# Kernel optimization log

Hardware: AMD Instinct MI355X
Metric: run time of the kernel (lower is better)

## Reference

```python
import jax, jax.numpy as jnp
import numpy as np

N = 8192
F_IN = 256
F_OUT = 256
S = 128          # state_dim
D_INNER = 512    # int(2.0 * out_features)


def _ln(x, g, b, eps=1e-5):
    m = x.mean(-1, keepdims=True)
    v = ((x - m) ** 2).mean(-1, keepdims=True)
    return (x - m) / jnp.sqrt(v + eps) * g + b


def setup_inputs() -> dict:
    key = jax.random.key(0)
    ks = jax.random.split(key, 20)
    s = 0.05
    d = {}
    d['h'] = jax.random.normal(ks[0], (N, F_IN), dtype=jnp.float32)
    d['adj'] = jax.random.randint(ks[1], (N, N), 0, 2, dtype=jnp.int32)
    d['W'] = jax.random.normal(ks[2], (F_IN, F_OUT), dtype=jnp.float32) * s
    d['a_src'] = jax.random.normal(ks[3], (F_OUT, 1), dtype=jnp.float32) * s
    d['a_dst'] = jax.random.normal(ks[4], (F_OUT, 1), dtype=jnp.float32) * s
    d['W_bcdt'] = jax.random.normal(ks[5], (F_OUT, 3 * S), dtype=jnp.float32) * s
    d['b_bcdt'] = jnp.zeros((3 * S,), jnp.float32)
    d['abp_w'] = jax.random.normal(ks[6], (S, F_OUT), dtype=jnp.float32) * s
    d['abp_b'] = jnp.zeros((F_OUT,), jnp.float32)
    d['cp_w'] = jax.random.normal(ks[7], (S, 1), dtype=jnp.float32) * s
    d['cp_b'] = jnp.zeros((1,), jnp.float32)
    d['W_hz'] = jax.random.normal(ks[8], (F_OUT, 2 * D_INNER), dtype=jnp.float32) * s
    d['b_hz'] = jnp.zeros((2 * D_INNER,), jnp.float32)
    d['out_w'] = jax.random.normal(ks[9], (D_INNER, F_OUT), dtype=jnp.float32) * s
    d['out_b'] = jnp.zeros((F_OUT,), jnp.float32)
    d['fe1_w'] = jax.random.normal(ks[10], (F_OUT, D_INNER), dtype=jnp.float32) * s
    d['fe1_b'] = jnp.zeros((D_INNER,), jnp.float32)
    d['fe_ln_g'] = jnp.ones((D_INNER,), jnp.float32)
    d['fe_ln_b'] = jnp.zeros((D_INNER,), jnp.float32)
    d['fe2_w'] = jax.random.normal(ks[11], (D_INNER, F_OUT), dtype=jnp.float32) * s
    d['fe2_b'] = jnp.zeros((F_OUT,), jnp.float32)
    d['A'] = jax.random.uniform(ks[12], (S,), minval=1.0, maxval=64.0, dtype=jnp.float32)
    d['D'] = jnp.ones((1,), jnp.float32)
    d['g1_w'] = jax.random.normal(ks[13], (2 * F_OUT, 2 * F_OUT), dtype=jnp.float32) * s
    d['g1_b'] = jnp.zeros((2 * F_OUT,), jnp.float32)
    d['g_ln_g'] = jnp.ones((2 * F_OUT,), jnp.float32)
    d['g_ln_b'] = jnp.zeros((2 * F_OUT,), jnp.float32)
    d['g2_w'] = jax.random.normal(ks[14], (2 * F_OUT, F_OUT), dtype=jnp.float32) * s
    d['g2_b'] = jnp.zeros((F_OUT,), jnp.float32)
    d['ln_g'] = jnp.ones((F_OUT,), jnp.float32)
    d['ln_b'] = jnp.zeros((F_OUT,), jnp.float32)
    return d


def reference(h, adj, W, a_src, a_dst, W_bcdt, b_bcdt, abp_w, abp_b, cp_w, cp_b,
              W_hz, b_hz, out_w, out_b, fe1_w, fe1_b, fe_ln_g, fe_ln_b, fe2_w,
              fe2_b, A, D, g1_w, g1_b, g_ln_g, g_ln_b, g2_w, g2_b, ln_g, ln_b):
    Wh = h @ W                                   # [N, F_OUT]
    # GAT-style masked attention
    e = Wh @ a_src + (Wh @ a_dst).T              # [N, N]
    e = jnp.where(e > 0, e, 0.2 * e)             # leaky_relu(0.2)
    e = jnp.where(adj > 0, e, jnp.float32(-9e15))
    attn = jax.nn.softmax(e, axis=1)
    h_attn = attn @ Wh                           # [N, F_OUT]
    # feature enhancer
    h_enh = jax.nn.silu(_ln(Wh @ fe1_w + fe1_b, fe_ln_g, fe_ln_b)) @ fe2_w + fe2_b
    # SSM-like branch
    BCdt = Wh @ W_bcdt + b_bcdt                  # [N, 3S]
    B, C, dt = jnp.split(BCdt, 3, axis=1)
    Asm = jax.nn.softmax(dt + A[None, :], axis=1)
    ab = (Asm * B) @ abp_w + abp_b               # [N, F_OUT]
    hs = Wh * ab
    hz = hs @ W_hz + b_hz                        # [N, 2*D_INNER]
    h_part, z = jnp.split(hz, 2, axis=1)
    hs = (h_part * jax.nn.silu(z) + h_part * D) @ out_w + out_b
    c_proj = C @ cp_w + cp_b                     # [N, 1]
    hs = hs * (1.0 + c_proj)
    # gated fusion
    comb = jnp.concatenate([h_attn, hs], axis=1)  # [N, 2*F_OUT]
    g = jax.nn.sigmoid(jax.nn.silu(_ln(comb @ g1_w + g1_b, g_ln_g, g_ln_b)) @ g2_w + g2_b)
    fused = g * h_attn + (1.0 - g) * hs + h_enh
    return _ln(fused, ln_g, ln_b)
```

## Files before the change

kernel.cpp:

```cpp
#include <hip/hip_runtime.h>
#include <cstdint>

typedef __attribute__((ext_vector_type(8))) short short8;
typedef __attribute__((ext_vector_type(4))) float f32x4;

#define DEVINL static __device__ __forceinline__

DEVINL ushort f2b(float f) {
    uint32_t u = __builtin_bit_cast(uint32_t, f);
    u += 0x7FFFu + ((u >> 16) & 1u);
    return (ushort)(u >> 16);
}

typedef __attribute__((address_space(3))) uint32_t lds_u32;
typedef const __attribute__((address_space(1))) uint32_t glb_u32;

DEVINL void load_lds_16(const ushort* g, ushort* l) {
    __builtin_amdgcn_global_load_lds((glb_u32*)g, (lds_u32*)l, 16, 0, 0);
}

constexpr int EPI_F32      = 0;
constexpr int EPI_MUL_BF16 = 2;
constexpr int EPI_SCALE_FB = 3;

template<int K, int EPI>
DEVINL void gemm_k_dev(
    const ushort* __restrict__ A, const ushort* __restrict__ BT,
    const float* __restrict__ bias, int N,
    float* __restrict__ outf, ushort* __restrict__ outb, int obld, int oboff,
    const float* __restrict__ extra, int bx, int by,
    ushort* Asm, ushort* Bsm)
{
    const int wave = threadIdx.x >> 6;
    const int lane = threadIdx.x & 63;
    const int quad = lane >> 4, l16 = lane & 15;
    const int lr = lane >> 3, ls = lane & 7;
    const int m0 = bx * 64, n0 = by * 64;

    f32x4 zero = {0.f, 0.f, 0.f, 0.f};
    f32x4 acc[4] = {zero, zero, zero, zero};

    for (int k0 = 0; k0 < K; k0 += 64) {
        #pragma unroll
        for (int p = 0; p < 2; ++p) {
            const int r = wave * 16 + p * 8 + lr;
            load_lds_16(A + (size_t)(m0 + r) * K + k0 + ((ls ^ (r & 7)) * 8),
                        Asm + (size_t)(wave * 16 + p * 8) * 64);
            load_lds_16(BT + (size_t)(n0 + r) * K + k0 + ((ls ^ (r & 7)) * 8),
                        Bsm + (size_t)(wave * 16 + p * 8) * 64);
        }
        __syncthreads();
        #pragma unroll
        for (int ks = 0; ks < 2; ++ks) {
            const int sl = ((ks * 4 + quad) ^ (l16 & 7)) * 8;
            short8 af = *(const short8*)(Asm + (wave * 16 + l16) * 64 + sl);
            #pragma unroll
            for (int c = 0; c < 4; ++c) {
                short8 bf = *(const short8*)(Bsm + (c * 16 + l16) * 64 + sl);
                acc[c] = __builtin_amdgcn_mfma_f32_16x16x32_bf16(af, bf, acc[c], 0, 0, 0);
            }
        }
        __syncthreads();
    }

    #pragma unroll
    for (int r = 0; r < 4; ++r) {
        const int row = m0 + wave * 16 + quad * 4 + r;
        #pragma unroll
        for (int c = 0; c < 4; ++c) {
            const int col = n0 + c * 16 + l16;
            float v = acc[c][r] + (bias ? bias[col] : 0.f);
            if (EPI == EPI_MUL_BF16) v *= extra[(size_t)row * N + col];
            if (EPI == EPI_SCALE_FB) v *= extra[row];
            if (EPI == EPI_F32 || EPI == EPI_SCALE_FB)
                outf[(size_t)row * N + col] = v;
            if (EPI == EPI_MUL_BF16 || EPI == EPI_SCALE_FB)
                outb[(size_t)row * obld + oboff + col] = f2b(v);
        }
    }
}

__global__ __launch_bounds__(256) void gemm_wh_kernel(
    const ushort* __restrict__ A, const ushort* __restrict__ BT,
    const float* __restrict__ asrc, const float* __restrict__ adst,
    float* __restrict__ Wh, ushort* __restrict__ Whbf, ushort* __restrict__ WhF,
    float* __restrict__ sOut, float* __restrict__ dOut)
{
    __shared__ ushort smem[2 * 64 * 64];
    ushort* Asm = smem;
    ushort* Bsm = smem + 4096;
    constexpr int K = 256;

    const int tid = threadIdx.x;
    const int wave = tid >> 6, lane = tid & 63;
    const int quad = lane >> 4, l16 = lane & 15;
    const int lr = lane >> 3, ls = lane & 7;
    const int m0 = blockIdx.x * 64, n0 = blockIdx.y * 64;

    f32x4 zero = {0.f, 0.f, 0.f, 0.f};
    f32x4 acc[4] = {zero, zero, zero, zero};

    for (int k0 = 0; k0 < K; k0 += 64) {
        #pragma unroll
        for (int p = 0; p < 2; ++p) {
            const int r = wave * 16 + p * 8 + lr;
            load_lds_16(A + (size_t)(m0 + r) * K + k0 + ((ls ^ (r & 7)) * 8),
                        Asm + (size_t)(wave * 16 + p * 8) * 64);
            load_lds_16(BT + (size_t)(n0 + r) * K + k0 + ((ls ^ (r & 7)) * 8),
                        Bsm + (size_t)(wave * 16 + p * 8) * 64);
        }
        __syncthreads();
        #pragma unroll
        for (int ks = 0; ks < 2; ++ks) {
            const int sl = ((ks * 4 + quad) ^ (l16 & 7)) * 8;
            short8 af = *(const short8*)(Asm + (wave * 16 + l16) * 64 + sl);
            #pragma unroll
            for (int c = 0; c < 4; ++c) {
                short8 bf = *(const short8*)(Bsm + (c * 16 + l16) * 64 + sl);
                acc[c] = __builtin_amdgcn_mfma_f32_16x16x32_bf16(af, bf, acc[c], 0, 0, 0);
            }
        }
        __syncthreads();
    }

    ushort* Tsm = smem;
    #pragma unroll
    for (int r = 0; r < 4; ++r) {
        const int rl = wave * 16 + quad * 4 + r;
        const int row = m0 + rl;
        float sp = 0.f, dp = 0.f;
        #pragma unroll
        for (int c = 0; c < 4; ++c) {
            const int cl = c * 16 + l16;
            const int col = n0 + cl;
            const float v = acc[c][r];
            Wh[(size_t)row * 256 + col] = v;
            const ushort b = f2b(v);
            Whbf[(size_t)row * 256 + col] = b;
            Tsm[cl * 72 + rl] = b;
            sp += v * asrc[col]; dp += v * adst[col];
        }
        #pragma unroll
        for (int o = 1; o < 16; o <<= 1) {
            sp += __shfl_xor(sp, o);
            dp += __shfl_xor(dp, o);
        }
        if (l16 == 0) {
            atomicAdd(&sOut[row], sp);
            atomicAdd(&dOut[row], dp);
        }
    }
    __syncthreads();
    const int jb0 = m0 >> 5, fb0 = n0 >> 4;
    #pragma unroll
    for (int jbl = 0; jbl < 2; ++jbl) {
        uint4 v = *(const uint4*)(Tsm + (wave * 16 + l16) * 72 + jbl * 32 + quad * 8);
        *(uint4*)(WhF + ((size_t)((jb0 + jbl) * 16 + fb0 + wave) * 64 + lane) * 8) = v;
    }
}

constexpr int EPR_LNSILU = 0;
constexpr int EPR_BCDT   = 1;
constexpr int EPR_HZ     = 2;
constexpr int EPR_FINAL  = 3;

template<int K, int N, int EPI>
DEVINL void gemm_row_dev(
    const ushort* __restrict__ A, const ushort* __restrict__ BT,
    const float* __restrict__ bias,
    float* __restrict__ outf, ushort* __restrict__ outb,
    const float* __restrict__ q0, const float* __restrict__ q1,
    const float* __restrict__ q2, const float* __restrict__ q3,
    const float* __restrict__ q4,
    int bx, int by, ushort* Asm, ushort* Bsm, float* red)
{
    constexpr int NW = N / 4;
    constexpr int NF = NW / 16;

    const int wave = threadIdx.x >> 6;
    const int lane = threadIdx.x & 63;
    const int quad = lane >> 4, l16 = lane & 15;
    const int lr = lane >> 3, ls = lane & 7;
    const int m0 = bx * 16;
    const ushort* Bb = BT + (EPI == EPR_HZ ? (size_t)by * 512 * K : 0);

    f32x4 zero = {0.f, 0.f, 0.f, 0.f};
    f32x4 acc[NF];
    #pragma unroll
    for (int c = 0; c < NF; ++c) acc[c] = zero;

    for (int k0 = 0; k0 < K; k0 += 64) {
        if (wave < 2) {
            const int r = wave * 8 + lr;
            load_lds_16(A + (size_t)(m0 + r) * K + k0 + ((ls ^ (r & 7)) * 8),
                        Asm + (size_t)(wave * 8) * 64);
        }
        #pragma unroll
        for (int p = 0; p < NW / 8; ++p) {
            const int n = wave * NW + p * 8 + lr;
            load_lds_16(Bb + (size_t)n * K + k0 + ((ls ^ (n & 7)) * 8),
                        Bsm + (size_t)(wave * NW + p * 8) * 64);
        }
        __syncthreads();
        #pragma unroll
        for (int ks = 0; ks < 2; ++ks) {
            const int sl = ((ks * 4 + quad) ^ (l16 & 7)) * 8;
            short8 af = *(const short8*)(Asm + l16 * 64 + sl);
            #pragma unroll
            for (int c = 0; c < NF; ++c) {
                const int gf = (EPI == EPR_BCDT) ? (wave + 4 * c) : (wave * NF + c);
                short8 bf = *(const short8*)(Bsm + (gf * 16 + l16) * 64 + sl);
                acc[c] = __builtin_amdgcn_mfma_f32_16x16x32_bf16(af, bf, acc[c], 0, 0, 0);
            }
        }
        __syncthreads();
    }

    if constexpr (EPI != EPR_HZ) {
        #pragma unroll
        for (int c = 0; c < NF; ++c) {
            const int gf = (EPI == EPR_BCDT) ? (wave + 4 * c) : (wave * NF + c);
            const float bs = bias[gf * 16 + l16];
            #pragma unroll
            for (int r = 0; r < 4; ++r) acc[c][r] += bs;
        }
    }

    if constexpr (EPI == EPR_LNSILU) {
        float s[4], q[4];
        #pragma unroll
        for (int r = 0; r < 4; ++r) {
            s[r] = 0.f; q[r] = 0.f;
            #pragma unroll
            for (int c = 0; c < NF; ++c) { const float v = acc[c][r]; s[r] += v; q[r] += v * v; }
            #pragma unroll
            for (int o = 1; o < 16; o <<= 1) { s[r] += __shfl_xor(s[r], o); q[r] += __shfl_xor(q[r], o); }
        }
        if (l16 == 0) {
            #pragma unroll
            for (int r = 0; r < 4; ++r) {
                red[(quad * 4 + r) * 8 + wave * 2]     = s[r];
                red[(quad * 4 + r) * 8 + wave * 2 + 1] = q[r];
            }
        }
        __syncthreads();
        #pragma unroll
        for (int r = 0; r < 4; ++r) {
            const int row16 = quad * 4 + r;
            float S = 0.f, Q = 0.f;
            #pragma unroll
            for (int w = 0; w < 4; ++w) { S += red[row16 * 8 + w * 2]; Q += red[row16 * 8 + w * 2 + 1]; }
            const float mean = S * (1.f / N);
            const float rstd = rsqrtf(Q * (1.f / N) - mean * mean + 1e-5f);
            #pragma unroll
            for (int c = 0; c < NF; ++c) {
                const int col = (wave * NF + c) * 16 + l16;
                const float y = (acc[c][r] - mean) * rstd * q0[col] + q1[col];
                outb[(size_t)(m0 + row16) * N + col] = f2b(y / (1.f + __expf(-y)));
            }
        }
    } else if constexpr (EPI == EPR_BCDT) {
        float t[2][4], e[2][4];
        #pragma unroll
        for (int ci = 0; ci < 2; ++ci) {
            const int dcol = (wave + 4 * (ci + 4)) * 16 - 256 + l16;
            const float av = q0[dcol];
            #pragma unroll
            for (int r = 0; r < 4; ++r) t[ci][r] = acc[ci + 4][r] + av;
        }
        float pm[4];
        #pragma unroll
        for (int r = 0; r < 4; ++r) {
            pm[r] = fmaxf(t[0][r], t[1][r]);
            #pragma unroll
            for (int o = 1; o < 16; o <<= 1) pm[r] = fmaxf(pm[r], __shfl_xor(pm[r], o));
        }
        if (l16 == 0) {
            #pragma unroll
            for (int r = 0; r < 4; ++r) red[(quad * 4 + r) * 4 + wave] = pm[r];
        }
        __syncthreads();
        float mx[4];
        #pragma unroll
        for (int r = 0; r < 4; ++r) {
            const int row16 = quad * 4 + r;
            mx[r] = fmaxf(fmaxf(red[row16 * 4], red[row16 * 4 + 1]),
                          fmaxf(red[row16 * 4 + 2], red[row16 * 4 + 3]));
        }
        float pe[4], pc2[4];
        #pragma unroll
        for (int r = 0; r < 4; ++r) {
            e[0][r] = __expf(t[0][r] - mx[r]);
            e[1][r] = __expf(t[1][r] - mx[r]);
            pe[r] = e[0][r] + e[1][r];
            pc2[r] = 0.f;
            #pragma unroll
            for (int ci = 0; ci < 2; ++ci) {
                const int ccol = (wave + 4 * (ci + 2)) * 16 - 128 + l16;
                pc2[r] += acc[ci + 2][r] * q1[ccol];
            }
            #pragma unroll
            for (int o = 1; o < 16; o <<= 1) { pe[r] += __shfl_xor(pe[r], o); pc2[r] += __shfl_xor(pc2[r], o); }
        }
        if (l16 == 0) {
            #pragma unroll
            for (int r = 0; r < 4; ++r) {
                red[64  + (quad * 4 + r) * 4 + wave] = pe[r];
                red[128 + (quad * 4 + r) * 4 + wave] = pc2[r];
            }
        }
        __syncthreads();
        #pragma unroll
        for (int r = 0; r < 4; ++r) {
            const int row16 = quad * 4 + r;
            const float inv = 1.f / (red[64 + row16 * 4] + red[64 + row16 * 4 + 1] +
                                     red[64 + row16 * 4 + 2] + red[64 + row16 * 4 + 3]);
            #pragma unroll
            for (int ci = 0; ci < 2; ++ci) {
                const int bcol = (wave + 4 * ci) * 16 + l16;
                outb[(size_t)(m0 + row16) * 128 + bcol] = f2b(acc[ci][r] * e[ci][r] * inv);
            }
        }
        if (wave == 0 && l16 == 0) {
            #pragma unroll
            for (int r = 0; r < 4; ++r) {
                const int row16 = quad * 4 + r;
                outf[m0 + row16] = 1.f + red[128 + row16 * 4] + red[128 + row16 * 4 + 1] +
                                   red[128 + row16 * 4 + 2] + red[128 + row16 * 4 + 3] + q2[0];
            }
        }
    } else if constexpr (EPI == EPR_HZ) {
        float* ep = (float*)Bsm;
        const float D0 = q0[0];
        if (wave >= 2) {
            #pragma unroll
            for (int c = 0; c < NF; ++c) {
                const int lc = (wave * NF + c) * 16 + l16;
                const float bz = bias[512 + by * 256 + lc - 256];
                #pragma unroll
                for (int r = 0; r < 4; ++r) {
                    const float z = acc[c][r] + bz;
                    ep[(quad * 4 + r) * 256 + lc - 256] = z / (1.f + __expf(-z)) + D0;
                }
            }
        }
        __syncthreads();
        if (wave < 2) {
            #pragma unroll
            for (int c = 0; c < NF; ++c) {
                const int lc = (wave * NF + c) * 16 + l16;
                const float bh = bias[by * 256 + lc];
                #pragma unroll
                for (int r = 0; r < 4; ++r) {
                    const float v = (acc[c][r] + bh) * ep[(quad * 4 + r) * 256 + lc];
                    outb[(size_t)(m0 + quad * 4 + r) * 512 + by * 256 + lc] = f2b(v);
                }
            }
        }
    } else {
        float fv[NF][4], s[4], q[4];
        #pragma unroll
        for (int r = 0; r < 4; ++r) { s[r] = 0.f; q[r] = 0.f; }
        #pragma unroll
        for (int c = 0; c < NF; ++c) {
            const int col = (wave * NF + c) * 16 + l16;
            #pragma unroll
            for (int r = 0; r < 4; ++r) {
                const size_t idx = (size_t)(m0 + quad * 4 + r) * 256 + col;
                const float g = 1.f / (1.f + __expf(-acc[c][r]));
                const float f = g * q0[idx] + (1.f - g) * q1[idx] + q2[idx];
                fv[c][r] = f; s[r] += f; q[r] += f * f;
            }
        }
        #pragma unroll
        for (int r = 0; r < 4; ++r) {
            #pragma unroll
            for (int o = 1; o < 16; o <<= 1) { s[r] += __shfl_xor(s[r], o); q[r] += __shfl_xor(q[r], o); }
        }
        if (l16 == 0) {
            #pragma unroll
            for (int r = 0; r < 4; ++r) {
                red[(quad * 4 + r) * 8 + wave * 2]     = s[r];
                red[(quad * 4 + r) * 8 + wave * 2 + 1] = q[r];
            }
        }
        __syncthreads();
        #pragma unroll
        for (int r = 0; r < 4; ++r) {
            const int row16 = quad * 4 + r;
            float S = 0.f, Q = 0.f;
            #pragma unroll
            for (int w = 0; w < 4; ++w) { S += red[row16 * 8 + w * 2]; Q += red[row16 * 8 + w * 2 + 1]; }
            const float mean = S * (1.f / 256.f);
            const float rstd = rsqrtf(Q * (1.f / 256.f) - mean * mean + 1e-5f);
            #pragma unroll
            for (int c = 0; c < NF; ++c) {
                const int col = (wave * NF + c) * 16 + l16;
                outf[(size_t)(m0 + row16) * 256 + col] = (fv[c][r] - mean) * rstd * q3[col] + q4[col];
            }
        }
    }
}

__global__ __launch_bounds__(256) void attn_kernel(
    const int* __restrict__ adj, const float* __restrict__ sA,
    const float* __restrict__ dA, const ushort* __restrict__ WhF,
    float* __restrict__ Upart, float* __restrict__ lpart)
{
    const int tid  = threadIdx.x;
    const int wave = tid >> 6, lane = tid & 63, quad = lane >> 4, l16 = lane & 15;
    const int i0 = blockIdx.x * 64;
    const int js = blockIdx.y;
    const int jbase = js * 2048;
    const int jb0 = jbase >> 5;
    const int rt = wave & 1, ch = wave >> 1;
    const int rr = lane >> 2, jg = lane & 3;
    const int row0 = i0 + rt * 32 + rr;
    const int row1 = row0 + 16;
    const float s0 = sA[row0], s1 = sA[row1];
    const int* adj0 = adj + (size_t)row0 * 8192 + jbase + jg * 8;
    const int* adj1 = adj + (size_t)row1 * 8192 + jbase + jg * 8;
    const float* dAp = dA + jbase + jg * 8;
    const int perm = ((l16 << 2) | quad) << 2;

    f32x4 zero = {0.f, 0.f, 0.f, 0.f};
    f32x4 acc[2][8] = {{zero, zero, zero, zero, zero, zero, zero, zero},
                       {zero, zero, zero, zero, zero, zero, zero, zero}};
    float ls0 = 0.f, ls1 = 0.f;

    #pragma unroll 2
    for (int cb = 0; cb < 64; ++cb) {
        const int off = cb * 32;
        const float4 d0 = *(const float4*)(dAp + off);
        const float4 d1 = *(const float4*)(dAp + off + 4);
        const int4 a00 = *(const int4*)(adj0 + off);
        const int4 a01 = *(const int4*)(adj0 + off + 4);
        const int4 a10 = *(const int4*)(adj1 + off);
        const int4 a11 = *(const int4*)(adj1 + off + 4);
        const float dd[8] = {d0.x, d0.y, d0.z, d0.w, d1.x, d1.y, d1.z, d1.w};
        const int aa0[8] = {a00.x, a00.y, a00.z, a00.w, a01.x, a01.y, a01.z, a01.w};
        const int aa1[8] = {a10.x, a10.y, a10.z, a10.w, a11.x, a11.y, a11.z, a11.w};
        ushort us0[8], us1[8];
        #pragma unroll
        for (int q = 0; q < 8; ++q) {
            float e0 = s0 + dd[q];
            e0 = fmaxf(e0, 0.2f * e0);
            const float w0 = aa0[q] ? __expf(e0) : 0.f;
            ls0 += w0; us0[q] = f2b(w0);
            float e1 = s1 + dd[q];
            e1 = fmaxf(e1, 0.2f * e1);
            const float w1 = aa1[q] ? __expf(e1) : 0.f;
            ls1 += w1; us1[q] = f2b(w1);
        }
        union FR { int d[4]; short8 v; } f0, f1;
        #pragma unroll
        for (int d = 0; d < 4; ++d) {
            const int p0 = (int)((uint)us0[2 * d] | ((uint)us0[2 * d + 1] << 16));
            const int p1 = (int)((uint)us1[2 * d] | ((uint)us1[2 * d + 1] << 16));
            f0.d[d] = __builtin_amdgcn_ds_bpermute(perm, p0);
            f1.d[d] = __builtin_amdgcn_ds_bpermute(perm, p1);
        }
        const ushort* Bp = WhF + ((size_t)((jb0 + cb) * 16 + ch * 8) * 64 + lane) * 8;
        #pragma unroll
        for (int c = 0; c < 8; ++c) {
            short8 bf = *(const short8*)(Bp + (size_t)c * 64 * 8);
            acc[0][c] = __builtin_amdgcn_mfma_f32_16x16x32_bf16(f0.v, bf, acc[0][c], 0, 0, 0);
            acc[1][c] = __builtin_amdgcn_mfma_f32_16x16x32_bf16(f1.v, bf, acc[1][c], 0, 0, 0);
        }
    }

    ls0 += __shfl_down(ls0, 1); ls0 += __shfl_down(ls0, 2);
    ls1 += __shfl_down(ls1, 1); ls1 += __shfl_down(ls1, 2);
    if (ch == 0 && jg == 0) {
        lpart[(size_t)js * 8192 + row0] = ls0;
        lpart[(size_t)js * 8192 + row1] = ls1;
    }

    #pragma unroll
    for (int it = 0; it < 2; ++it) {
        #pragma unroll
        for (int c = 0; c < 8; ++c) {
            const int col = ch * 128 + c * 16 + l16;
            #pragma unroll
            for (int r = 0; r < 4; ++r) {
                const int row = i0 + rt * 32 + it * 16 + quad * 4 + r;
                Upart[((size_t)js * 8192 + row) * 256 + col] = acc[it][c][r];
            }
        }
    }
}

__global__ __launch_bounds__(256) void post_attn_kernel(
    const float* __restrict__ Upart, const float* __restrict__ lpart,
    float* __restrict__ hattn, ushort* __restrict__ comb,
    const ushort* __restrict__ Whbf,
    const ushort* __restrict__ fe1T, const float* __restrict__ fe1_b,
    const float* __restrict__ fe_ln_g, const float* __restrict__ fe_ln_b,
    ushort* __restrict__ tact,
    const ushort* __restrict__ bcdtT, const float* __restrict__ b_bcdt,
    const float* __restrict__ Avec, const float* __restrict__ cpw,
    const float* __restrict__ cpb,
    ushort* __restrict__ SB, float* __restrict__ cscl)
{
    __shared__ ushort Asm[16 * 64];
    __shared__ ushort Bsm[512 * 64];
    __shared__ float red[192];
    const int b = blockIdx.x;

    if (b < 2048) {
        const int row = b * 4 + (threadIdx.x >> 6);
        const int lane = threadIdx.x & 63;
        float l = 0.f;
        #pragma unroll
        for (int js = 0; js < 4; ++js) l += lpart[(size_t)js * 8192 + row];
        const float inv = 1.f / l;
        float4 u = {0.f, 0.f, 0.f, 0.f};
        #pragma unroll
        for (int js = 0; js < 4; ++js) {
            const float4 t = *(const float4*)&Upart[((size_t)js * 8192 + row) * 256 + lane * 4];
            u.x += t.x; u.y += t.y; u.z += t.z; u.w += t.w;
        }
        u.x *= inv; u.y *= inv; u.z *= inv; u.w *= inv;
        *(float4*)&hattn[(size_t)row * 256 + lane * 4] = u;
        union { ushort us[4]; uint2 v; } pk;
        pk.us[0] = f2b(u.x); pk.us[1] = f2b(u.y); pk.us[2] = f2b(u.z); pk.us[3] = f2b(u.w);
        *(uint2*)&comb[(size_t)row * 512 + lane * 4] = pk.v;
    } else if (b < 2560) {
        gemm_row_dev<256, 512, EPR_LNSILU>(Whbf, fe1T, fe1_b, nullptr, tact,
            fe_ln_g, fe_ln_b, nullptr, nullptr, nullptr, b - 2048, 0, Asm, Bsm, red);
    } else {
        gemm_row_dev<256, 384, EPR_BCDT>(Whbf, bcdtT, b_bcdt, cscl, SB,
            Avec, cpw, cpb, nullptr, nullptr, b - 2560, 0, Asm, Bsm, red);
    }
}

__global__ __launch_bounds__(256) void gemm_fe2_sb_kernel(
    const ushort* __restrict__ tact, const ushort* __restrict__ fe2T,
    const float* __restrict__ fe2_b, float* __restrict__ henh,
    const ushort* __restrict__ SB, const ushort* __restrict__ abpT,
    const float* __restrict__ abp_b, ushort* __restrict__ hsbf,
    const float* __restrict__ Wh)
{
    __shared__ ushort Asm[64 * 64];
    __shared__ ushort Bsm[64 * 64];
    const int b = blockIdx.x;
    if (b < 512)
        gemm_k_dev<512, EPI_F32>(tact, fe2T, fe2_b, 256, henh, nullptr, 0, 0,
                                 nullptr, b & 127, b >> 7, Asm, Bsm);
    else
        gemm_k_dev<128, EPI_MUL_BF16>(SB, abpT, abp_b, 256, nullptr, hsbf, 256, 0,
                                      Wh, (b - 512) & 127, (b - 512) >> 7, Asm, Bsm);
}

__global__ __launch_bounds__(256) void gemm_hz_kernel(
    const ushort* __restrict__ hsbf, const ushort* __restrict__ hzT,
    const float* __restrict__ b_hz, ushort* __restrict__ vbf,
    const float* __restrict__ Dvec)
{
    __shared__ ushort Asm[16 * 64];
    __shared__ ushort Bsm[512 * 64];
    __shared__ float red[192];
    gemm_row_dev<256, 512, EPR_HZ>(hsbf, hzT, b_hz, nullptr, vbf, Dvec,
        nullptr, nullptr, nullptr, nullptr, blockIdx.x, blockIdx.y, Asm, Bsm, red);
}

__global__ __launch_bounds__(256) void gemm_out_kernel(
    const ushort* __restrict__ vbf, const ushort* __restrict__ outT,
    const float* __restrict__ out_b, float* __restrict__ hs2,
    ushort* __restrict__ comb, const float* __restrict__ cscl)
{
    __shared__ ushort Asm[64 * 64];
    __shared__ ushort Bsm[64 * 64];
    gemm_k_dev<512, EPI_SCALE_FB>(vbf, outT, out_b, 256, hs2, comb, 512, 256,
                                  cscl, blockIdx.x, blockIdx.y, Asm, Bsm);
}

__global__ __launch_bounds__(256) void gemm_g1_kernel(
    const ushort* __restrict__ comb, const ushort* __restrict__ g1T,
    const float* __restrict__ g1_b, ushort* __restrict__ tact,
    const float* __restrict__ g_ln_g, const float* __restrict__ g_ln_b)
{
    __shared__ ushort Asm[16 * 64];
    __shared__ ushort Bsm[512 * 64];
    __shared__ float red[192];
    gemm_row_dev<512, 512, EPR_LNSILU>(comb, g1T, g1_b, nullptr, tact,
        g_ln_g, g_ln_b, nullptr, nullptr, nullptr, blockIdx.x, 0, Asm, Bsm, red);
}

__global__ __launch_bounds__(256) void gemm_final_kernel(
    const ushort* __restrict__ tact, const ushort* __restrict__ g2T,
    const float* __restrict__ g2_b, float* __restrict__ outp,
    const float* __restrict__ hattn, const float* __restrict__ hs2,
    const float* __restrict__ henh, const float* __restrict__ ln_g,
    const float* __restrict__ ln_b)
{
    __shared__ ushort Asm[16 * 64];
    __shared__ ushort Bsm[256 * 64];
    __shared__ float red[192];
    gemm_row_dev<512, 256, EPR_FINAL>(tact, g2T, g2_b, outp, nullptr,
        hattn, hs2, henh, ln_g, ln_b, blockIdx.x, 0, Asm, Bsm, red);
}

struct TJob { const float* in; ushort* out; int R, C, off, perm; };
struct TArgs { TJob j[10]; };

DEVINL int hzperm(int j) {
    return (j < 512) ? ((j >> 8) << 9) + (j & 255)
                     : (((j - 512) >> 8) << 9) + 256 + ((j - 512) & 255);
}

__global__ __launch_bounds__(256) void multi_transpose_kernel(TArgs a)
{
    __shared__ float tile[32][33];
    const int b = blockIdx.x;
    int ji = 0;
    #pragma unroll
    for (int k = 1; k < 10; ++k) if (b >= a.j[k].off) ji = k;
    const TJob J = a.j[ji];
    const int t = b - J.off;

    if (J.R == 0) {
        const int base = t * 1024 + threadIdx.x;
        #pragma unroll
        for (int k = 0; k < 4; ++k)
            J.out[base + k * 256] = f2b(J.in[base + k * 256]);
        return;
    }
    const int CB = J.C >> 5;
    const int bx = t % CB, by = t / CB;
    const int tx = threadIdx.x & 31, ty = threadIdx.x >> 5;
    const int c0 = bx * 32, r0 = by * 32;
    #pragma unroll
    for (int i = ty; i < 32; i += 8)
        tile[i][tx] = J.in[(size_t)(r0 + i) * J.C + (c0 + tx)];
    __syncthreads();
    #pragma unroll
    for (int i = ty; i < 32; i += 8) {
        int orow = c0 + i;
        if (J.perm) orow = hzperm(orow);
        J.out[(size_t)orow * J.R + (r0 + tx)] = f2b(tile[tx][i]);
    }
}

extern "C" void kernel_launch(void* const* d_in, const int* in_sizes, int n_in,
                              void* d_out, int out_size, void* d_ws, size_t ws_size,
                              hipStream_t stream)
{
    const float* h      = (const float*)d_in[0];
    const int*   adj    = (const int*)  d_in[1];
    const float* W      = (const float*)d_in[2];
    const float* a_src  = (const float*)d_in[3];
    const float* a_dst  = (const float*)d_in[4];
    const float* W_bcdt = (const float*)d_in[5];
    const float* b_bcdt = (const float*)d_in[6];
    const float* abp_w  = (const float*)d_in[7];
    const float* abp_b  = (const float*)d_in[8];
    const float* cp_w   = (const float*)d_in[9];
    const float* cp_b   = (const float*)d_in[10];
    const float* W_hz   = (const float*)d_in[11];
    const float* b_hz   = (const float*)d_in[12];
    const float* out_w  = (const float*)d_in[13];
    const float* out_b  = (const float*)d_in[14];
    const float* fe1_w  = (const float*)d_in[15];
    const float* fe1_b  = (const float*)d_in[16];
    const float* fe_ln_g= (const float*)d_in[17];
    const float* fe_ln_b= (const float*)d_in[18];
    const float* fe2_w  = (const float*)d_in[19];
    const float* fe2_b  = (const float*)d_in[20];
    const float* Avec   = (const float*)d_in[21];
    const float* Dvec   = (const float*)d_in[22];
    const float* g1_w   = (const float*)d_in[23];
    const float* g1_b   = (const float*)d_in[24];
    const float* g_ln_g = (const float*)d_in[25];
    const float* g_ln_b = (const float*)d_in[26];
    const float* g2_w   = (const float*)d_in[27];
    const float* g2_b   = (const float*)d_in[28];
    const float* ln_g   = (const float*)d_in[29];
    const float* ln_b   = (const float*)d_in[30];
    float* outp = (float*)d_out;

    char* p = (char*)d_ws;
    size_t off = 0;
    auto take = [&](size_t nbytes) -> void* {
        void* r = p + off;
        off += (nbytes + 255) & ~(size_t)255;
        return r;
    };
    ushort* wT    = (ushort*)take(256 * 256 * 2);
    ushort* fe1T  = (ushort*)take(512 * 256 * 2);
    ushort* fe2T  = (ushort*)take(256 * 512 * 2);
    ushort* bcdtT = (ushort*)take(384 * 256 * 2);
    ushort* hzT   = (ushort*)take(1024 * 256 * 2);
    ushort* outT  = (ushort*)take(256 * 512 * 2);
    ushort* g1T   = (ushort*)take(512 * 512 * 2);
    ushort* g2T   = (ushort*)take(256 * 512 * 2);
    ushort* abpT  = (ushort*)take(256 * 128 * 2);
    ushort* hbf   = (ushort*)take((size_t)8192 * 256 * 2);
    float*  Wh    = (float*) take((size_t)8192 * 256 * 4);
    ushort* Whbf  = (ushort*)take((size_t)8192 * 256 * 2);
    ushort* WhF   = (ushort*)take((size_t)8192 * 256 * 2);
    float*  sbuf  = (float*) take(8192 * 4);
    float*  dbuf  = (float*) take(8192 * 4);
    float*  cscl  = (float*) take(8192 * 4);
    float*  hattn = (float*) take((size_t)8192 * 256 * 4);
    float*  henh  = (float*) take((size_t)8192 * 256 * 4);
    float*  lpart = (float*) take(4 * 8192 * 4);
    ushort* SB    = (ushort*)take((size_t)8192 * 128 * 2);
    ushort* hsbf  = (ushort*)take((size_t)8192 * 256 * 2);
    ushort* vbf   = (ushort*)take((size_t)8192 * 512 * 2);
    float*  hs2   = (float*) take((size_t)8192 * 256 * 4);
    ushort* comb  = (ushort*)take((size_t)8192 * 512 * 2);
    ushort* tact  = (ushort*)take((size_t)8192 * 512 * 2);
    float*  Upart = (float*) take((size_t)4 * 8192 * 256 * 4);

    (void)in_sizes; (void)n_in; (void)out_size; (void)ws_size;

    hipMemsetAsync(sbuf, 0, 2 * 8192 * sizeof(float), stream);

    {
        TArgs ta; int boff = 0;
        auto addT = [&](int i, const float* in, ushort* out, int R, int C, int perm) {
            ta.j[i] = TJob{in, out, R, C, boff, perm};
            boff += (R / 32) * (C / 32);
        };
        addT(0, W,      wT,    256, 256,  0);
        addT(1, fe1_w,  fe1T,  256, 512,  0);
        addT(2, fe2_w,  fe2T,  512, 256,  0);
        addT(3, W_bcdt, bcdtT, 256, 384,  0);
        addT(4, abp_w,  abpT,  128, 256,  0);
        addT(5, W_hz,   hzT,   256, 1024, 1);
        addT(6, out_w,  outT,  512, 256,  0);
        addT(7, g1_w,   g1T,   512, 512,  0);
        addT(8, g2_w,   g2T,   512, 256,  0);
        ta.j[9] = TJob{h, hbf, 0, 8192 * 256, boff, 0};
        boff += (8192 * 256) / 1024;
        multi_transpose_kernel<<<boff, 256, 0, stream>>>(ta);
    }

    gemm_wh_kernel<<<dim3(128, 4), 256, 0, stream>>>(
        hbf, wT, a_src, a_dst, Wh, Whbf, WhF, sbuf, dbuf);

    attn_kernel<<<dim3(128, 4), 256, 0, stream>>>(adj, sbuf, dbuf, WhF, Upart, lpart);

    post_attn_kernel<<<3072, 256, 0, stream>>>(
        Upart, lpart, hattn, comb, Whbf,
        fe1T, fe1_b, fe_ln_g, fe_ln_b, tact,
        bcdtT, b_bcdt, Avec, cp_w, cp_b, SB, cscl);

    gemm_fe2_sb_kernel<<<1024, 256, 0, stream>>>(
        tact, fe2T, fe2_b, henh, SB, abpT, abp_b, hsbf, Wh);

    gemm_hz_kernel<<<dim3(512, 2), 256, 0, stream>>>(hsbf, hzT, b_hz, vbf, Dvec);

    gemm_out_kernel<<<dim3(128, 4), 256, 0, stream>>>(vbf, outT, out_b, hs2, comb, cscl);

    gemm_g1_kernel<<<512, 256, 0, stream>>>(comb, g1T, g1_b, tact, g_ln_g, g_ln_b);

    gemm_final_kernel<<<512, 256, 0, stream>>>(
        tact, g2T, g2_b, outp, hattn, hs2, henh, ln_g, ln_b);
}
```

Measured before the change: 614.5 us.

## Co-schedule attention with fe1/BCdt GEMMs and store attention partials in bf16

Attention blocks now run in the same launch as the independent fe1 and BCdt row GEMMs, interleaved by block index, so the adjacency-bound attention work can overlap with compute-bound GEMM work. The partial-sum reduction moves into the following fe2/SB kernel. Per-split attention partial accumulators are written as bf16 instead of fp32, halving that intermediate traffic. The cost is reduced precision in the partial sums and a larger static LDS footprint for the attention blocks, which may lower occupancy.

Measured after the change: 676.7 us. 1.1x slower.

```diff
diff --git a/kernel.cpp b/kernel.cpp
--- a/kernel.cpp
+++ b/kernel.cpp
@@ -10,6 +10,10 @@
     uint32_t u = __builtin_bit_cast(uint32_t, f);
     u += 0x7FFFu + ((u >> 16) & 1u);
     return (ushort)(u >> 16);
+}
+DEVINL float b2f(ushort u) {
+    uint32_t x = (uint32_t)u << 16;
+    return __builtin_bit_cast(float, x);
 }
 
 typedef __attribute__((address_space(3))) uint32_t lds_u32;
@@ -402,15 +406,15 @@
     }
 }
 
-__global__ __launch_bounds__(256) void attn_kernel(
+DEVINL void attn_dev(
     const int* __restrict__ adj, const float* __restrict__ sA,
     const float* __restrict__ dA, const ushort* __restrict__ WhF,
-    float* __restrict__ Upart, float* __restrict__ lpart)
+    ushort* __restrict__ Upart, float* __restrict__ lpart,
+    int bx, int js)
 {
     const int tid  = threadIdx.x;
     const int wave = tid >> 6, lane = tid & 63, quad = lane >> 4, l16 = lane & 15;
-    const int i0 = blockIdx.x * 64;
-    const int js = blockIdx.y;
+    const int i0 = bx * 64;
     const int jbase = js * 2048;
     const int jb0 = jbase >> 5;
     const int rt = wave & 1, ch = wave >> 1;
@@ -484,15 +488,16 @@
             #pragma unroll
             for (int r = 0; r < 4; ++r) {
                 const int row = i0 + rt * 32 + it * 16 + quad * 4 + r;
-                Upart[((size_t)js * 8192 + row) * 256 + col] = acc[it][c][r];
-            }
-        }
-    }
-}
-
-__global__ __launch_bounds__(256) void post_attn_kernel(
-    const float* __restrict__ Upart, const float* __restrict__ lpart,
-    float* __restrict__ hattn, ushort* __restrict__ comb,
+                Upart[((size_t)js * 8192 + row) * 256 + col] = f2b(acc[it][c][r]);
+            }
+        }
+    }
+}
+
+__global__ __launch_bounds__(256) void mega_kernel(
+    const int* __restrict__ adj, const float* __restrict__ sbuf,
+    const float* __restrict__ dbuf, const ushort* __restrict__ WhF,
+    ushort* __restrict__ Upart, float* __restrict__ lpart,
     const ushort* __restrict__ Whbf,
     const ushort* __restrict__ fe1T, const float* __restrict__ fe1_b,
     const float* __restrict__ fe_ln_g, const float* __restrict__ fe_ln_b,
@@ -506,35 +511,23 @@
     __shared__ ushort Bsm[512 * 64];
     __shared__ float red[192];
     const int b = blockIdx.x;
-
-    if (b < 2048) {
-        const int row = b * 4 + (threadIdx.x >> 6);
-        const int lane = threadIdx.x & 63;
-        float l = 0.f;
-        #pragma unroll
-        for (int js = 0; js < 4; ++js) l += lpart[(size_t)js * 8192 + row];
-        const float inv = 1.f / l;
-        float4 u = {0.f, 0.f, 0.f, 0.f};
-        #pragma unroll
-        for (int js = 0; js < 4; ++js) {
-            const float4 t = *(const float4*)&Upart[((size_t)js * 8192 + row) * 256 + lane * 4];
-            u.x += t.x; u.y += t.y; u.z += t.z; u.w += t.w;
-        }
-        u.x *= inv; u.y *= inv; u.z *= inv; u.w *= inv;
-        *(float4*)&hattn[(size_t)row * 256 + lane * 4] = u;
-        union { ushort us[4]; uint2 v; } pk;
-        pk.us[0] = f2b(u.x); pk.us[1] = f2b(u.y); pk.us[2] = f2b(u.z); pk.us[3] = f2b(u.w);
-        *(uint2*)&comb[(size_t)row * 512 + lane * 4] = pk.v;
-    } else if (b < 2560) {
+    const int type = b % 3;
+    const int idx = b / 3;
+
+    if (type == 0) {
+        attn_dev(adj, sbuf, dbuf, WhF, Upart, lpart, idx & 127, idx >> 7);
+    } else if (type == 1) {
         gemm_row_dev<256, 512, EPR_LNSILU>(Whbf, fe1T, fe1_b, nullptr, tact,
-            fe_ln_g, fe_ln_b, nullptr, nullptr, nullptr, b - 2048, 0, Asm, Bsm, red);
+            fe_ln_g, fe_ln_b, nullptr, nullptr, nullptr, idx, 0, Asm, Bsm, red);
     } else {
         gemm_row_dev<256, 384, EPR_BCDT>(Whbf, bcdtT, b_bcdt, cscl, SB,
-            Avec, cpw, cpb, nullptr, nullptr, b - 2560, 0, Asm, Bsm, red);
-    }
-}
-
-__global__ __launch_bounds__(256) void gemm_fe2_sb_kernel(
+            Avec, cpw, cpb, nullptr, nullptr, idx, 0, Asm, Bsm, red);
+    }
+}
+
+__global__ __launch_bounds__(256) void c2_kernel(
+    const ushort* __restrict__ Upart, const float* __restrict__ lpart,
+    float* __restrict__ hattn, ushort* __restrict__ comb,
     const ushort* __restrict__ tact, const ushort* __restrict__ fe2T,
     const float* __restrict__ fe2_b, float* __restrict__ henh,
     const ushort* __restrict__ SB, const ushort* __restrict__ abpT,
@@ -544,12 +537,37 @@
     __shared__ ushort Asm[64 * 64];
     __shared__ ushort Bsm[64 * 64];
     const int b = blockIdx.x;
-    if (b < 512)
+
+    if (b < 2048) {
+        const int row = b * 4 + (threadIdx.x >> 6);
+        const int lane = threadIdx.x & 63;
+        float l = 0.f;
+        #pragma unroll
+        for (int js = 0; js < 4; ++js) l += lpart[(size_t)js * 8192 + row];
+        const float inv = 1.f / l;
+        float u[4] = {0.f, 0.f, 0.f, 0.f};
+        #pragma unroll
+        for (int js = 0; js < 4; ++js) {
+            union { ushort us[4]; uint2 v; } t;
+            t.v = *(const uint2*)&Upart[((size_t)js * 8192 + row) * 256 + lane * 4];
+            #pragma unroll
+            for (int k = 0; k < 4; ++k) u[k] += b2f(t.us[k]);
+        }
+        union { ushort us[4]; uint2 v; } pk;
+        float4 uf;
+        uf.x = u[0] * inv; uf.y = u[1] * inv; uf.z = u[2] * inv; uf.w = u[3] * inv;
+        *(float4*)&hattn[(size_t)row * 256 + lane * 4] = uf;
+        pk.us[0] = f2b(uf.x); pk.us[1] = f2b(uf.y); pk.us[2] = f2b(uf.z); pk.us[3] = f2b(uf.w);
+        *(uint2*)&comb[(size_t)row * 512 + lane * 4] = pk.v;
+    } else if (b < 2560) {
+        const int t = b - 2048;
         gemm_k_dev<512, EPI_F32>(tact, fe2T, fe2_b, 256, henh, nullptr, 0, 0,
-                                 nullptr, b & 127, b >> 7, Asm, Bsm);
-    else
+                                 nullptr, t & 127, t >> 7, Asm, Bsm);
+    } else {
+        const int t = b - 2560;
         gemm_k_dev<128, EPI_MUL_BF16>(SB, abpT, abp_b, 256, nullptr, hsbf, 256, 0,
-                                      Wh, (b - 512) & 127, (b - 512) >> 7, Asm, Bsm);
+                                      Wh, t & 127, t >> 7, Asm, Bsm);
+    }
 }
 
 __global__ __launch_bounds__(256) void gemm_hz_kernel(
@@ -711,7 +729,7 @@
     float*  hs2   = (float*) take((size_t)8192 * 256 * 4);
     ushort* comb  = (ushort*)take((size_t)8192 * 512 * 2);
     ushort* tact  = (ushort*)take((size_t)8192 * 512 * 2);
-    float*  Upart = (float*) take((size_t)4 * 8192 * 256 * 4);
+    ushort* Upart = (ushort*)take((size_t)4 * 8192 * 256 * 2);
 
     (void)in_sizes; (void)n_in; (void)out_size; (void)ws_size;
 
@@ -740,14 +758,13 @@
     gemm_wh_kernel<<<dim3(128, 4), 256, 0, stream>>>(
         hbf, wT, a_src, a_dst, Wh, Whbf, WhF, sbuf, dbuf);
 
-    attn_kernel<<<dim3(128, 4), 256, 0, stream>>>(adj, sbuf, dbuf, WhF, Upart, lpart);
-
-    post_attn_kernel<<<3072, 256, 0, stream>>>(
-        Upart, lpart, hattn, comb, Whbf,
-        fe1T, fe1_b, fe_ln_g, fe_ln_b, tact,
+    mega_kernel<<<1536, 256, 0, stream>>>(
+        adj, sbuf, dbuf, WhF, Upart, lpart,
+        Whbf, fe1T, fe1_b, fe_ln_g, fe_ln_b, tact,
         bcdtT, b_bcdt, Avec, cp_w, cp_b, SB, cscl);
 
-    gemm_fe2_sb_kernel<<<1024, 256, 0, stream>>>(
+    c2_kernel<<<3072, 256, 0, stream>>>(
+        Upart, lpart, hattn, comb,
         tact, fe2T, fe2_b, henh, SB, abpT, abp_b, hsbf, Wh);
 
     gemm_hz_kernel<<<dim3(512, 2), 256, 0, stream>>>(hsbf, hzT, b_hz, vbf, Dvec);
```

## Pack adjacency into bitmask and store attention partials in bf16

Applied to the files above, without the earlier changes.

Adds a pre-pass in the transpose kernel that converts the int32 adjacency matrix into a bitmask laid out for the attention kernel's access pattern. The attention kernel then reads one byte per 8 neighbours instead of 32 bytes. The partial attention sums are written as bf16 instead of fp32, halving that intermediate traffic. The cost is an extra full read of adj in the pack pass and a loss of precision in the partial sums before normalization.

Measured after the change: 628.4 us. 1.02x slower.

```diff
diff --git a/kernel.cpp b/kernel.cpp
--- a/kernel.cpp
+++ b/kernel.cpp
@@ -10,6 +10,10 @@
     uint32_t u = __builtin_bit_cast(uint32_t, f);
     u += 0x7FFFu + ((u >> 16) & 1u);
     return (ushort)(u >> 16);
+}
+DEVINL float b2f(ushort u) {
+    uint32_t x = (uint32_t)u << 16;
+    return __builtin_bit_cast(float, x);
 }
 
 typedef __attribute__((address_space(3))) uint32_t lds_u32;
@@ -403,9 +407,9 @@
 }
 
 __global__ __launch_bounds__(256) void attn_kernel(
-    const int* __restrict__ adj, const float* __restrict__ sA,
+    const uchar* __restrict__ pmask, const float* __restrict__ sA,
     const float* __restrict__ dA, const ushort* __restrict__ WhF,
-    float* __restrict__ Upart, float* __restrict__ lpart)
+    ushort* __restrict__ Upart, float* __restrict__ lpart)
 {
     const int tid  = threadIdx.x;
     const int wave = tid >> 6, lane = tid & 63, quad = lane >> 4, l16 = lane & 15;
@@ -418,8 +422,8 @@
     const int row0 = i0 + rt * 32 + rr;
     const int row1 = row0 + 16;
     const float s0 = sA[row0], s1 = sA[row1];
-    const int* adj0 = adj + (size_t)row0 * 8192 + jbase + jg * 8;
-    const int* adj1 = adj + (size_t)row1 * 8192 + jbase + jg * 8;
+    const uchar* pm0 = pmask + ((size_t)(row0 * 4 + js) * 4 + jg) * 64;
+    const uchar* pm1 = pmask + ((size_t)(row1 * 4 + js) * 4 + jg) * 64;
     const float* dAp = dA + jbase + jg * 8;
     const int perm = ((l16 << 2) | quad) << 2;
 
@@ -433,23 +437,19 @@
         const int off = cb * 32;
         const float4 d0 = *(const float4*)(dAp + off);
         const float4 d1 = *(const float4*)(dAp + off + 4);
-        const int4 a00 = *(const int4*)(adj0 + off);
-        const int4 a01 = *(const int4*)(adj0 + off + 4);
-        const int4 a10 = *(const int4*)(adj1 + off);
-        const int4 a11 = *(const int4*)(adj1 + off + 4);
+        const uint mb0 = pm0[cb];
+        const uint mb1 = pm1[cb];
         const float dd[8] = {d0.x, d0.y, d0.z, d0.w, d1.x, d1.y, d1.z, d1.w};
-        const int aa0[8] = {a00.x, a00.y, a00.z, a00.w, a01.x, a01.y, a01.z, a01.w};
-        const int aa1[8] = {a10.x, a10.y, a10.z, a10.w, a11.x, a11.y, a11.z, a11.w};
         ushort us0[8], us1[8];
         #pragma unroll
         for (int q = 0; q < 8; ++q) {
             float e0 = s0 + dd[q];
             e0 = fmaxf(e0, 0.2f * e0);
-            const float w0 = aa0[q] ? __expf(e0) : 0.f;
+            const float w0 = ((mb0 >> q) & 1u) ? __expf(e0) : 0.f;
             ls0 += w0; us0[q] = f2b(w0);
             float e1 = s1 + dd[q];
             e1 = fmaxf(e1, 0.2f * e1);
-            const float w1 = aa1[q] ? __expf(e1) : 0.f;
+            const float w1 = ((mb1 >> q) & 1u) ? __expf(e1) : 0.f;
             ls1 += w1; us1[q] = f2b(w1);
         }
         union FR { int d[4]; short8 v; } f0, f1;
@@ -484,14 +484,14 @@
             #pragma unroll
             for (int r = 0; r < 4; ++r) {
                 const int row = i0 + rt * 32 + it * 16 + quad * 4 + r;
-                Upart[((size_t)js * 8192 + row) * 256 + col] = acc[it][c][r];
+                Upart[((size_t)js * 8192 + row) * 256 + col] = f2b(acc[it][c][r]);
             }
         }
     }
 }
 
 __global__ __launch_bounds__(256) void post_attn_kernel(
-    const float* __restrict__ Upart, const float* __restrict__ lpart,
+    const ushort* __restrict__ Upart, const float* __restrict__ lpart,
     float* __restrict__ hattn, ushort* __restrict__ comb,
     const ushort* __restrict__ Whbf,
     const ushort* __restrict__ fe1T, const float* __restrict__ fe1_b,
@@ -514,16 +514,19 @@
         #pragma unroll
         for (int js = 0; js < 4; ++js) l += lpart[(size_t)js * 8192 + row];
         const float inv = 1.f / l;
-        float4 u = {0.f, 0.f, 0.f, 0.f};
+        float u[4] = {0.f, 0.f, 0.f, 0.f};
         #pragma unroll
         for (int js = 0; js < 4; ++js) {
-            const float4 t = *(const float4*)&Upart[((size_t)js * 8192 + row) * 256 + lane * 4];
-            u.x += t.x; u.y += t.y; u.z += t.z; u.w += t.w;
-        }
-        u.x *= inv; u.y *= inv; u.z *= inv; u.w *= inv;
-        *(float4*)&hattn[(size_t)row * 256 + lane * 4] = u;
+            union { ushort us[4]; uint2 v; } t;
+            t.v = *(const uint2*)&Upart[((size_t)js * 8192 + row) * 256 + lane * 4];
+            #pragma unroll
+            for (int k = 0; k < 4; ++k) u[k] += b2f(t.us[k]);
+        }
+        float4 uf;
+        uf.x = u[0] * inv; uf.y = u[1] * inv; uf.z = u[2] * inv; uf.w = u[3] * inv;
+        *(float4*)&hattn[(size_t)row * 256 + lane * 4] = uf;
         union { ushort us[4]; uint2 v; } pk;
-        pk.us[0] = f2b(u.x); pk.us[1] = f2b(u.y); pk.us[2] = f2b(u.z); pk.us[3] = f2b(u.w);
+        pk.us[0] = f2b(uf.x); pk.us[1] = f2b(uf.y); pk.us[2] = f2b(uf.z); pk.us[3] = f2b(uf.w);
         *(uint2*)&comb[(size_t)row * 512 + lane * 4] = pk.v;
     } else if (b < 2560) {
         gemm_row_dev<256, 512, EPR_LNSILU>(Whbf, fe1T, fe1_b, nullptr, tact,
@@ -602,7 +605,7 @@
 }
 
 struct TJob { const float* in; ushort* out; int R, C, off, perm; };
-struct TArgs { TJob j[10]; };
+struct TArgs { TJob j[11]; };
 
 DEVINL int hzperm(int j) {
     return (j < 512) ? ((j >> 8) << 9) + (j & 255)
@@ -615,10 +618,41 @@
     const int b = blockIdx.x;
     int ji = 0;
     #pragma unroll
-    for (int k = 1; k < 10; ++k) if (b >= a.j[k].off) ji = k;
+    for (int k = 1; k < 11; ++k) if (b >= a.j[k].off) ji = k;
     const TJob J = a.j[ji];
     const int t = b - J.off;
 
+    if (J.R == -1) {
+        const int* ap = (const int*)J.in;
+        uchar* pm = (uchar*)tile;
+        const int wrow = threadIdx.x >> 6;
+        const int sub  = threadIdx.x & 63;
+        const int row = t * 4 + wrow;
+        #pragma unroll
+        for (int i = 0; i < 16; ++i) {
+            const int byteidx = i * 64 + sub;
+            const int j0 = byteidx * 8;
+            const int4 v0 = *(const int4*)(ap + (size_t)row * 8192 + j0);
+            const int4 v1 = *(const int4*)(ap + (size_t)row * 8192 + j0 + 4);
+            uint bb = 0;
+            bb |= (v0.x != 0) ? 1u : 0u;
+            bb |= (v0.y != 0) ? 2u : 0u;
+            bb |= (v0.z != 0) ? 4u : 0u;
+            bb |= (v0.w != 0) ? 8u : 0u;
+            bb |= (v1.x != 0) ? 16u : 0u;
+            bb |= (v1.y != 0) ? 32u : 0u;
+            bb |= (v1.z != 0) ? 64u : 0u;
+            bb |= (v1.w != 0) ? 128u : 0u;
+            const int js = byteidx >> 8, rem = byteidx & 255;
+            const int cb = rem >> 2, jg = rem & 3;
+            pm[wrow * 1024 + ((js * 4 + jg) << 6) + cb] = (uchar)bb;
+        }
+        __syncthreads();
+        const uint4* src = (const uint4*)tile;
+        uint4* dst = (uint4*)((uchar*)J.out + (size_t)t * 4096);
+        dst[threadIdx.x] = src[threadIdx.x];
+        return;
+    }
     if (J.R == 0) {
         const int base = t * 1024 + threadIdx.x;
         #pragma unroll
@@ -699,6 +733,7 @@
     float*  Wh    = (float*) take((size_t)8192 * 256 * 4);
     ushort* Whbf  = (ushort*)take((size_t)8192 * 256 * 2);
     ushort* WhF   = (ushort*)take((size_t)8192 * 256 * 2);
+    uchar*  pmask = (uchar*) take((size_t)8192 * 1024);
     float*  sbuf  = (float*) take(8192 * 4);
     float*  dbuf  = (float*) take(8192 * 4);
     float*  cscl  = (float*) take(8192 * 4);
@@ -711,7 +746,7 @@
     float*  hs2   = (float*) take((size_t)8192 * 256 * 4);
     ushort* comb  = (ushort*)take((size_t)8192 * 512 * 2);
     ushort* tact  = (ushort*)take((size_t)8192 * 512 * 2);
-    float*  Upart = (float*) take((size_t)4 * 8192 * 256 * 4);
+    ushort* Upart = (ushort*)take((size_t)4 * 8192 * 256 * 2);
 
     (void)in_sizes; (void)n_in; (void)out_size; (void)ws_size;
 
@@ -734,13 +769,15 @@
         addT(8, g2_w,   g2T,   512, 256,  0);
         ta.j[9] = TJob{h, hbf, 0, 8192 * 256, boff, 0};
         boff += (8192 * 256) / 1024;
+        ta.j[10] = TJob{(const float*)adj, (ushort*)pmask, -1, 0, boff, 0};
+        boff += 8192 / 4;
         multi_transpose_kernel<<<boff, 256, 0, stream>>>(ta);
     }
 
     gemm_wh_kernel<<<dim3(128, 4), 256, 0, stream>>>(
         hbf, wT, a_src, a_dst, Wh, Whbf, WhF, sbuf, dbuf);
 
-    attn_kernel<<<dim3(128, 4), 256, 0, stream>>>(adj, sbuf, dbuf, WhF, Upart, lpart);
+    attn_kernel<<<dim3(128, 4), 256, 0, stream>>>(pmask, sbuf, dbuf, WhF, Upart, lpart);
 
     post_attn_kernel<<<3072, 256, 0, stream>>>(
         Upart, lpart, hattn, comb, Whbf,
```
